# Kernel tuning notes

Measured on AMD Instinct MI355X. Metric: run time of the kernel, lower is better.

The kernel has to match this reference:

```python
import jax, jax.numpy as jnp
import numpy as np

NUM_WIRES = 14
LAYERS = 3
PPL = 3
BATCH = 1024
DIM = 2 ** NUM_WIRES


def setup_inputs() -> dict:
    key = jax.random.key(0)
    k1, k2, k3, k4, k5 = jax.random.split(key, 5)
    sr = jax.random.normal(k1, (BATCH, DIM), jnp.float32)
    si = jax.random.normal(k2, (BATCH, DIM), jnp.float32)
    norm = jnp.sqrt(jnp.sum(sr * sr + si * si, axis=1, keepdims=True))
    sr, si = sr / norm, si / norm  # normalized amplitude-encoded states
    weights = jax.random.normal(k3, (LAYERS, PPL, NUM_WIRES), jnp.float32)
    head_w = jax.random.normal(k4, (1, NUM_WIRES), jnp.float32) / np.sqrt(NUM_WIRES)
    head_b = jax.random.normal(k5, (1,), jnp.float32) * 0.01
    return {"state_real": sr, "state_imag": si, "weights": weights,
            "head_w": head_w, "head_b": head_b}


def _apply_ry_all(st, angles):
    # st: (B,)+(2,)*n complex; apply RY(angles[q]) on each wire q (RYs on distinct wires commute)
    half = angles * 0.5
    c, s = jnp.cos(half), jnp.sin(half)
    for q in range(NUM_WIRES):
        ax = 1 + q
        a0 = jnp.take(st, 0, axis=ax)
        a1 = jnp.take(st, 1, axis=ax)
        n0 = c[q] * a0 - s[q] * a1
        n1 = s[q] * a0 + c[q] * a1
        st = jnp.stack([n0, n1], axis=ax)
    return st


def _apply_cnot(st, ctrl, tgt):
    # flip target axis only where control bit == 1
    ctrl_ax, tgt_ax = 1 + ctrl, 1 + tgt
    flipped = jnp.flip(st, axis=tgt_ax)
    mask_shape = [1] * (NUM_WIRES + 1)
    mask_shape[ctrl_ax] = 2
    mask = (jnp.arange(2).reshape(mask_shape) == 1)
    return jnp.where(mask, flipped, st)


def _circuit(state, weights):
    # state: (B, DIM) complex64 -> PauliZ expvals (B, NUM_WIRES)
    st = state.reshape((-1,) + (2,) * NUM_WIRES)
    for l in range(LAYERS):
        # sequential RY(w[l,p,q]) for p=0..PPL-1 on wire q compose to RY(sum_p w[l,p,q])
        ang = jnp.sum(weights[l], axis=0)  # (NUM_WIRES,)
        st = _apply_ry_all(st, ang)
        for j in range(NUM_WIRES):
            st = _apply_cnot(st, j, (j + 1) % NUM_WIRES)
    probs = st.real ** 2 + st.imag ** 2  # (B,)+(2,)*n
    probs = probs.reshape(-1, DIM)
    idx = jnp.arange(DIM)
    # PennyLane convention: wire 0 is the most significant bit
    bits = (idx[None, :] >> (NUM_WIRES - 1 - jnp.arange(NUM_WIRES))[:, None]) & 1  # (n, DIM)
    signs = (1 - 2 * bits).astype(probs.dtype)
    return probs @ signs.T  # (B, n)


def reference(state_real, state_imag, weights, head_w, head_b):
    state = jax.lax.complex(state_real, state_imag)
    feats = _circuit(state, weights)  # (B, NUM_WIRES)
    return feats @ head_w[0] + head_b[0]  # (B,)
```

## Files before the change

kernel.cpp:

```cpp
#include <hip/hip_runtime.h>

typedef unsigned int u32;

#define DIM 16384
#define NT  512

__host__ __device__ constexpr u32 swz0(u32 d) {
    u32 b1 = (d >> 4) & 1u;
    u32 b2 = (d >> 7) & 1u;
    u32 b3 = ((d >> 6) ^ (d >> 8)) & 1u;
    return d ^ (b1 << 1) ^ (b2 << 2) ^ (b3 << 3);
}

__host__ __device__ constexpr u32 mmap(u32 y) {
    u32 s = y;
    s ^= s >> 1; s ^= s >> 2; s ^= s >> 4; s ^= s >> 8;
    return (s & 0x1FFFu) | (((s ^ (y >> 13)) & 1u) << 13);
}

__device__ __forceinline__ void rot2(float2& a0, float2& a1, float c, float s) {
    float t0x = s * a1.x, t0y = s * a1.y;
    float t1x = s * a0.x, t1y = s * a0.y;
    float n0x = fmaf(c, a0.x, -t0x), n0y = fmaf(c, a0.y, -t0y);
    float n1x = fmaf(c, a1.x,  t1x), n1y = fmaf(c, a1.y,  t1y);
    a0.x = n0x; a0.y = n0y;
    a1.x = n1x; a1.y = n1y;
}

template<int D>
__device__ __forceinline__ void gate32(float2 (&am)[32], float c, float s) {
    #pragma unroll
    for (int r = 0; r < 32; ++r) if (!(r & D)) rot2(am[r], am[r | D], c, s);
}

template<int L>
__device__ __forceinline__ void passA(int tid, float* smem, float2 (&am)[32]) {
    float4* stv = (float4*)smem;
    const float* angC = smem + 32768;
    const float* angS = smem + 32768 + 48;
    u32 sbase = swz0((u32)tid << 2);
    if (L > 0) {
        #pragma unroll
        for (int h = 0; h < 8; ++h) {
            #pragma unroll
            for (int m = 0; m < 2; ++m) {
                u32 idx = (sbase ^ swz0(((u32)h << 11) | ((u32)m << 1))) >> 1;
                float4 v = stv[idx];
                int r = h * 4 + m * 2;
                am[r]     = make_float2(v.x, v.y);
                am[r + 1] = make_float2(v.z, v.w);
            }
        }
    }
    gate32< 1>(am, angC[L * 16 +  0], angS[L * 16 +  0]);
    gate32< 2>(am, angC[L * 16 +  1], angS[L * 16 +  1]);
    gate32< 4>(am, angC[L * 16 + 11], angS[L * 16 + 11]);
    gate32< 8>(am, angC[L * 16 + 12], angS[L * 16 + 12]);
    gate32<16>(am, angC[L * 16 + 13], angS[L * 16 + 13]);
    #pragma unroll
    for (int h = 0; h < 8; ++h) {
        #pragma unroll
        for (int m = 0; m < 2; ++m) {
            u32 idx = (sbase ^ swz0(((u32)h << 11) | ((u32)m << 1))) >> 1;
            int r = h * 4 + m * 2;
            stv[idx] = make_float4(am[r].x, am[r].y, am[r + 1].x, am[r + 1].y);
        }
    }
    __syncthreads();
}

template<int L>
__device__ __forceinline__ void passB(int tid, float* smem, float2 (&am)[32]) {
    float2* st2 = (float2*)smem;
    const float* angC = smem + 32768;
    const float* angS = smem + 32768 + 48;
    u32 ybase = ((u32)tid & 63u) | (((u32)tid >> 6) << 11);
    u32 sbase = swz0(ybase);
    #pragma unroll
    for (int j = 0; j < 32; ++j) am[j] = st2[sbase ^ swz0((u32)j << 6)];
    gate32< 1>(am, angC[L * 16 +  6], angS[L * 16 +  6]);
    gate32< 2>(am, angC[L * 16 +  7], angS[L * 16 +  7]);
    gate32< 4>(am, angC[L * 16 +  8], angS[L * 16 +  8]);
    gate32< 8>(am, angC[L * 16 +  9], angS[L * 16 +  9]);
    gate32<16>(am, angC[L * 16 + 10], angS[L * 16 + 10]);
    #pragma unroll
    for (int j = 0; j < 32; ++j) st2[sbase ^ swz0((u32)j << 6)] = am[j];
    __syncthreads();
}

template<int L>
__device__ __forceinline__ void passC(int tid, float* smem, float2 (&am)[32],
                                      float& acc, float W0) {
    float2* st2 = (float2*)smem;
    float4* stv = (float4*)smem;
    const float* angC  = smem + 32768;
    const float* angS  = smem + 32768 + 48;
    const float* lutLo = smem + 32768 + 96;
    const float* lutHi = smem + 32768 + 96 + 128;
    u32 ybase = (((u32)tid & 1u) << 1) | (((u32)tid >> 1) << 6);
    u32 sbase = swz0(ybase);
    #pragma unroll
    for (int h = 0; h < 16; ++h) {
        u32 idx = (sbase ^ swz0((u32)h << 2)) >> 1;
        float4 v = stv[idx];
        int r = h * 2;
        am[r]     = make_float2(v.x, v.y);
        am[r + 1] = make_float2(v.z, v.w);
    }
    gate32< 2>(am, angC[L * 16 + 2], angS[L * 16 + 2]);
    gate32< 4>(am, angC[L * 16 + 3], angS[L * 16 + 3]);
    gate32< 8>(am, angC[L * 16 + 4], angS[L * 16 + 4]);
    gate32<16>(am, angC[L * 16 + 5], angS[L * 16 + 5]);
    if (L < 2) {
        __syncthreads();
        u32 pbase = swz0(mmap(ybase));
        #pragma unroll
        for (int h = 0; h < 16; ++h) {
            #pragma unroll
            for (int q = 0; q < 2; ++q) {
                u32 slot = pbase ^ swz0(mmap(((u32)h << 2) | (u32)q));
                st2[slot] = am[h * 2 + q];
            }
        }
        __syncthreads();
    } else {
        u32 myb = mmap(ybase);
        #pragma unroll
        for (int h = 0; h < 16; ++h) {
            #pragma unroll
            for (int q = 0; q < 2; ++q) {
                u32 yp = myb ^ mmap(((u32)h << 2) | (u32)q);
                int r = h * 2 + q;
                float p  = fmaf(am[r].x, am[r].x, am[r].y * am[r].y);
                float wv = W0 - 2.0f * (lutLo[yp & 127u] + lutHi[yp >> 7]);
                acc = fmaf(wv, p, acc);
            }
        }
    }
}

__global__ __launch_bounds__(NT, 2) void qsim_kernel(
    const float* __restrict__ sreal, const float* __restrict__ simag,
    const float* __restrict__ wts,   const float* __restrict__ hw,
    const float* __restrict__ hb,    float* __restrict__ out)
{
    extern __shared__ float smem[];
    float* angC   = smem + 32768;
    float* angS   = angC + 48;
    float* lutLo  = angS + 48;
    float* lutHi  = lutLo + 128;
    float* redbuf = lutHi + 128;

    int tid = threadIdx.x;
    int b   = blockIdx.x;

    const float4* pr = (const float4*)(sreal + (size_t)b * DIM);
    const float4* pi = (const float4*)(simag + (size_t)b * DIM);
    float4 vr[8], vi[8];
    #pragma unroll
    for (int h = 0; h < 8; ++h) {
        vr[h] = pr[(h << 9) | tid];
        vi[h] = pi[(h << 9) | tid];
    }

    if (tid < 42) {
        int l = tid / 14, bb = tid % 14, q = 13 - bb;
        float a = 0.5f * (wts[l * 42 + q] + wts[l * 42 + 14 + q] + wts[l * 42 + 28 + q]);
        angC[l * 16 + bb] = cosf(a);
        angS[l * 16 + bb] = sinf(a);
    } else if (tid >= 64 && tid < 192) {
        int i = tid - 64;
        float ssum = 0.f;
        for (int bb = 0; bb < 7; ++bb) if ((i >> bb) & 1) ssum += hw[13 - bb];
        lutLo[i] = ssum;
    } else if (tid >= 192 && tid < 320) {
        int i = tid - 192;
        float ssum = 0.f;
        for (int bb = 0; bb < 7; ++bb) if ((i >> bb) & 1) ssum += hw[6 - bb];
        lutHi[i] = ssum;
    }

    float2 am[32];
    #pragma unroll
    for (int h = 0; h < 8; ++h) {
        am[h * 4 + 0] = make_float2(vr[h].x, vi[h].x);
        am[h * 4 + 1] = make_float2(vr[h].y, vi[h].y);
        am[h * 4 + 2] = make_float2(vr[h].z, vi[h].z);
        am[h * 4 + 3] = make_float2(vr[h].w, vi[h].w);
    }

    __syncthreads();
    float W0  = lutLo[127] + lutHi[127];
    float acc = 0.f;

    passA<0>(tid, smem, am);
    passB<0>(tid, smem, am);
    passC<0>(tid, smem, am, acc, W0);
    passA<1>(tid, smem, am);
    passB<1>(tid, smem, am);
    passC<1>(tid, smem, am, acc, W0);
    passA<2>(tid, smem, am);
    passB<2>(tid, smem, am);
    passC<2>(tid, smem, am, acc, W0);

    #pragma unroll
    for (int off = 32; off > 0; off >>= 1) acc += __shfl_xor(acc, off, 64);
    if ((tid & 63) == 0) redbuf[tid >> 6] = acc;
    __syncthreads();
    if (tid == 0) {
        float tot = hb[0];
        #pragma unroll
        for (int i = 0; i < 8; ++i) tot += redbuf[i];
        out[b] = tot;
    }
}

extern "C" void kernel_launch(void* const* d_in, const int* in_sizes, int n_in,
                              void* d_out, int out_size, void* d_ws, size_t ws_size,
                              hipStream_t stream)
{
    const float* sreal = (const float*)d_in[0];
    const float* simag = (const float*)d_in[1];
    const float* wts   = (const float*)d_in[2];
    const float* hw    = (const float*)d_in[3];
    const float* hb    = (const float*)d_in[4];
    float* out = (float*)d_out;

    int batch = in_sizes[0] / DIM;
    size_t smem_bytes = (32768 + 48 + 48 + 128 + 128 + 16) * sizeof(float);

    (void)hipFuncSetAttribute((const void*)qsim_kernel,
                              hipFuncAttributeMaxDynamicSharedMemorySize, (int)smem_bytes);
    qsim_kernel<<<dim3(batch), dim3(NT), smem_bytes, stream>>>(sreal, simag, wts, hw, hb, out);
}
```

Measured before the change: 211.7 us.

## Process two batch states per block, interleaving gate math with LDS shuffles

Each block now handles two batch rows. It alternates them so one state's register gate math overlaps the other's shared-memory transpose phases, and the batch grid is halved. The rotation math moves to packed v_pk_mul/v_pk_fma instructions on float pairs. The cost is twice the register state per thread, with 64 float2 amplitudes under launch_bounds(512,2), which risks spills. It also adds many more __syncthreads barriers and fewer blocks.

```diff
diff --git a/kernel.cpp b/kernel.cpp
--- a/kernel.cpp
+++ b/kernel.cpp
@@ -1,6 +1,7 @@
 #include <hip/hip_runtime.h>
 
 typedef unsigned int u32;
+typedef float v2f __attribute__((ext_vector_type(2)));
 
 #define DIM 16384
 #define NT  512
@@ -18,131 +19,142 @@
     return (s & 0x1FFFu) | (((s ^ (y >> 13)) & 1u) << 13);
 }
 
-__device__ __forceinline__ void rot2(float2& a0, float2& a1, float c, float s) {
-    float t0x = s * a1.x, t0y = s * a1.y;
-    float t1x = s * a0.x, t1y = s * a0.y;
-    float n0x = fmaf(c, a0.x, -t0x), n0y = fmaf(c, a0.y, -t0y);
-    float n1x = fmaf(c, a1.x,  t1x), n1y = fmaf(c, a1.y,  t1y);
-    a0.x = n0x; a0.y = n0y;
-    a1.x = n1x; a1.y = n1y;
+__device__ __forceinline__ v2f mkv2(float x, float y) { v2f t; t.x = x; t.y = y; return t; }
+
+__device__ __forceinline__ v2f pk_mul(v2f a, v2f b) {
+    v2f d;
+    asm("v_pk_mul_f32 %0, %1, %2" : "=v"(d) : "v"(a), "v"(b));
+    return d;
+}
+__device__ __forceinline__ v2f pk_fma(v2f a, v2f b, v2f c) {
+    v2f d;
+    asm("v_pk_fma_f32 %0, %1, %2, %3" : "=v"(d) : "v"(a), "v"(b), "v"(c));
+    return d;
+}
+
+__device__ __forceinline__ void rot2(v2f& a0, v2f& a1, v2f cc, v2f ss, v2f ns) {
+    v2f t1 = pk_mul(ss, a0);
+    v2f t0 = pk_mul(ns, a1);
+    a0 = pk_fma(cc, a0, t0);
+    a1 = pk_fma(cc, a1, t1);
 }
 
 template<int D>
-__device__ __forceinline__ void gate32(float2 (&am)[32], float c, float s) {
-    #pragma unroll
-    for (int r = 0; r < 32; ++r) if (!(r & D)) rot2(am[r], am[r | D], c, s);
-}
-
+__device__ __forceinline__ void gate32(v2f (&am)[32], float c, float s) {
+    v2f cc = {c, c}, ss = {s, s}, ns = {-s, -s};
+    #pragma unroll
+    for (int r = 0; r < 32; ++r) if (!(r & D)) rot2(am[r], am[r | D], cc, ss, ns);
+}
+
+__device__ __forceinline__ void rdA(int tid, float* smem, v2f (&am)[32]) {
+    float4* stv = (float4*)smem;
+    u32 sbase = swz0((u32)tid << 2);
+    #pragma unroll
+    for (int h = 0; h < 8; ++h)
+        #pragma unroll
+        for (int m = 0; m < 2; ++m) {
+            u32 idx = (sbase ^ swz0(((u32)h << 11) | ((u32)m << 1))) >> 1;
+            float4 v = stv[idx];
+            int r = h * 4 + m * 2;
+            am[r]     = mkv2(v.x, v.y);
+            am[r + 1] = mkv2(v.z, v.w);
+        }
+}
+__device__ __forceinline__ void wrA(int tid, float* smem, v2f (&am)[32]) {
+    float4* stv = (float4*)smem;
+    u32 sbase = swz0((u32)tid << 2);
+    #pragma unroll
+    for (int h = 0; h < 8; ++h)
+        #pragma unroll
+        for (int m = 0; m < 2; ++m) {
+            u32 idx = (sbase ^ swz0(((u32)h << 11) | ((u32)m << 1))) >> 1;
+            int r = h * 4 + m * 2;
+            stv[idx] = make_float4(am[r].x, am[r].y, am[r + 1].x, am[r + 1].y);
+        }
+}
 template<int L>
-__device__ __forceinline__ void passA(int tid, float* smem, float2 (&am)[32]) {
-    float4* stv = (float4*)smem;
-    const float* angC = smem + 32768;
-    const float* angS = smem + 32768 + 48;
-    u32 sbase = swz0((u32)tid << 2);
-    if (L > 0) {
-        #pragma unroll
-        for (int h = 0; h < 8; ++h) {
-            #pragma unroll
-            for (int m = 0; m < 2; ++m) {
-                u32 idx = (sbase ^ swz0(((u32)h << 11) | ((u32)m << 1))) >> 1;
-                float4 v = stv[idx];
-                int r = h * 4 + m * 2;
-                am[r]     = make_float2(v.x, v.y);
-                am[r + 1] = make_float2(v.z, v.w);
-            }
-        }
-    }
+__device__ __forceinline__ void gatesA(const float* angC, const float* angS, v2f (&am)[32]) {
     gate32< 1>(am, angC[L * 16 +  0], angS[L * 16 +  0]);
     gate32< 2>(am, angC[L * 16 +  1], angS[L * 16 +  1]);
     gate32< 4>(am, angC[L * 16 + 11], angS[L * 16 + 11]);
     gate32< 8>(am, angC[L * 16 + 12], angS[L * 16 + 12]);
     gate32<16>(am, angC[L * 16 + 13], angS[L * 16 + 13]);
-    #pragma unroll
-    for (int h = 0; h < 8; ++h) {
-        #pragma unroll
-        for (int m = 0; m < 2; ++m) {
-            u32 idx = (sbase ^ swz0(((u32)h << 11) | ((u32)m << 1))) >> 1;
-            int r = h * 4 + m * 2;
-            stv[idx] = make_float4(am[r].x, am[r].y, am[r + 1].x, am[r + 1].y);
-        }
-    }
-    __syncthreads();
-}
-
-template<int L>
-__device__ __forceinline__ void passB(int tid, float* smem, float2 (&am)[32]) {
-    float2* st2 = (float2*)smem;
-    const float* angC = smem + 32768;
-    const float* angS = smem + 32768 + 48;
+}
+
+__device__ __forceinline__ void rdB(int tid, float* smem, v2f (&am)[32]) {
+    v2f* st2 = (v2f*)smem;
     u32 ybase = ((u32)tid & 63u) | (((u32)tid >> 6) << 11);
     u32 sbase = swz0(ybase);
     #pragma unroll
     for (int j = 0; j < 32; ++j) am[j] = st2[sbase ^ swz0((u32)j << 6)];
+}
+__device__ __forceinline__ void wrB(int tid, float* smem, v2f (&am)[32]) {
+    v2f* st2 = (v2f*)smem;
+    u32 ybase = ((u32)tid & 63u) | (((u32)tid >> 6) << 11);
+    u32 sbase = swz0(ybase);
+    #pragma unroll
+    for (int j = 0; j < 32; ++j) st2[sbase ^ swz0((u32)j << 6)] = am[j];
+}
+template<int L>
+__device__ __forceinline__ void gatesB(const float* angC, const float* angS, v2f (&am)[32]) {
     gate32< 1>(am, angC[L * 16 +  6], angS[L * 16 +  6]);
     gate32< 2>(am, angC[L * 16 +  7], angS[L * 16 +  7]);
     gate32< 4>(am, angC[L * 16 +  8], angS[L * 16 +  8]);
     gate32< 8>(am, angC[L * 16 +  9], angS[L * 16 +  9]);
     gate32<16>(am, angC[L * 16 + 10], angS[L * 16 + 10]);
-    #pragma unroll
-    for (int j = 0; j < 32; ++j) st2[sbase ^ swz0((u32)j << 6)] = am[j];
-    __syncthreads();
-}
-
-template<int L>
-__device__ __forceinline__ void passC(int tid, float* smem, float2 (&am)[32],
-                                      float& acc, float W0) {
-    float2* st2 = (float2*)smem;
+}
+
+__device__ __forceinline__ void rdC(int tid, float* smem, v2f (&am)[32]) {
     float4* stv = (float4*)smem;
-    const float* angC  = smem + 32768;
-    const float* angS  = smem + 32768 + 48;
-    const float* lutLo = smem + 32768 + 96;
-    const float* lutHi = smem + 32768 + 96 + 128;
     u32 ybase = (((u32)tid & 1u) << 1) | (((u32)tid >> 1) << 6);
     u32 sbase = swz0(ybase);
     #pragma unroll
     for (int h = 0; h < 16; ++h) {
         u32 idx = (sbase ^ swz0((u32)h << 2)) >> 1;
         float4 v = stv[idx];
-        int r = h * 2;
-        am[r]     = make_float2(v.x, v.y);
-        am[r + 1] = make_float2(v.z, v.w);
-    }
+        am[h * 2]     = mkv2(v.x, v.y);
+        am[h * 2 + 1] = mkv2(v.z, v.w);
+    }
+}
+__device__ __forceinline__ void wrCs(int tid, float* smem, v2f (&am)[32]) {
+    v2f* st2 = (v2f*)smem;
+    u32 ybase = (((u32)tid & 1u) << 1) | (((u32)tid >> 1) << 6);
+    u32 pbase = swz0(mmap(ybase));
+    #pragma unroll
+    for (int h = 0; h < 16; ++h)
+        #pragma unroll
+        for (int q = 0; q < 2; ++q) {
+            u32 slot = pbase ^ swz0(mmap(((u32)h << 2) | (u32)q));
+            st2[slot] = am[h * 2 + q];
+        }
+}
+template<int L>
+__device__ __forceinline__ void gatesC(const float* angC, const float* angS, v2f (&am)[32]) {
     gate32< 2>(am, angC[L * 16 + 2], angS[L * 16 + 2]);
     gate32< 4>(am, angC[L * 16 + 3], angS[L * 16 + 3]);
     gate32< 8>(am, angC[L * 16 + 4], angS[L * 16 + 4]);
     gate32<16>(am, angC[L * 16 + 5], angS[L * 16 + 5]);
-    if (L < 2) {
-        __syncthreads();
-        u32 pbase = swz0(mmap(ybase));
-        #pragma unroll
-        for (int h = 0; h < 16; ++h) {
-            #pragma unroll
-            for (int q = 0; q < 2; ++q) {
-                u32 slot = pbase ^ swz0(mmap(((u32)h << 2) | (u32)q));
-                st2[slot] = am[h * 2 + q];
-            }
-        }
-        __syncthreads();
-    } else {
-        u32 myb = mmap(ybase);
-        #pragma unroll
-        for (int h = 0; h < 16; ++h) {
-            #pragma unroll
-            for (int q = 0; q < 2; ++q) {
-                u32 yp = myb ^ mmap(((u32)h << 2) | (u32)q);
-                int r = h * 2 + q;
-                float p  = fmaf(am[r].x, am[r].x, am[r].y * am[r].y);
-                float wv = W0 - 2.0f * (lutLo[yp & 127u] + lutHi[yp >> 7]);
-                acc = fmaf(wv, p, acc);
-            }
-        }
-    }
+}
+__device__ __forceinline__ void measC(int tid, const float* lutLo, const float* lutHi,
+                                      v2f (&am)[32], float& acc, float W0) {
+    u32 ybase = (((u32)tid & 1u) << 1) | (((u32)tid >> 1) << 6);
+    u32 myb = mmap(ybase);
+    #pragma unroll
+    for (int h = 0; h < 16; ++h)
+        #pragma unroll
+        for (int q = 0; q < 2; ++q) {
+            u32 yp = myb ^ mmap(((u32)h << 2) | (u32)q);
+            int r = h * 2 + q;
+            float p  = fmaf(am[r].x, am[r].x, am[r].y * am[r].y);
+            float wv = W0 - 2.0f * (lutLo[yp & 127u] + lutHi[yp >> 7]);
+            acc = fmaf(wv, p, acc);
+        }
 }
 
 __global__ __launch_bounds__(NT, 2) void qsim_kernel(
     const float* __restrict__ sreal, const float* __restrict__ simag,
     const float* __restrict__ wts,   const float* __restrict__ hw,
-    const float* __restrict__ hb,    float* __restrict__ out)
+    const float* __restrict__ hb,    float* __restrict__ out, int batch)
 {
     extern __shared__ float smem[];
     float* angC   = smem + 32768;
@@ -152,15 +164,23 @@
     float* redbuf = lutHi + 128;
 
     int tid = threadIdx.x;
-    int b   = blockIdx.x;
-
-    const float4* pr = (const float4*)(sreal + (size_t)b * DIM);
-    const float4* pi = (const float4*)(simag + (size_t)b * DIM);
-    float4 vr[8], vi[8];
-    #pragma unroll
-    for (int h = 0; h < 8; ++h) {
-        vr[h] = pr[(h << 9) | tid];
-        vi[h] = pi[(h << 9) | tid];
+    int b0  = blockIdx.x * 2;
+    int b1  = (b0 + 1 < batch) ? b0 + 1 : b0;
+
+    v2f am[32], bm[32];
+
+    {
+        const float4* pr = (const float4*)(sreal + (size_t)b0 * DIM);
+        const float4* pi = (const float4*)(simag + (size_t)b0 * DIM);
+        #pragma unroll
+        for (int h = 0; h < 8; ++h) {
+            float4 r = pr[(h << 9) | tid];
+            float4 i = pi[(h << 9) | tid];
+            am[h * 4 + 0] = mkv2(r.x, i.x);
+            am[h * 4 + 1] = mkv2(r.y, i.y);
+            am[h * 4 + 2] = mkv2(r.z, i.z);
+            am[h * 4 + 3] = mkv2(r.w, i.w);
+        }
     }
 
     if (tid < 42) {
@@ -180,38 +200,80 @@
         lutHi[i] = ssum;
     }
 
-    float2 am[32];
-    #pragma unroll
-    for (int h = 0; h < 8; ++h) {
-        am[h * 4 + 0] = make_float2(vr[h].x, vi[h].x);
-        am[h * 4 + 1] = make_float2(vr[h].y, vi[h].y);
-        am[h * 4 + 2] = make_float2(vr[h].z, vi[h].z);
-        am[h * 4 + 3] = make_float2(vr[h].w, vi[h].w);
+    {
+        const float4* pr = (const float4*)(sreal + (size_t)b1 * DIM);
+        const float4* pi = (const float4*)(simag + (size_t)b1 * DIM);
+        #pragma unroll
+        for (int h = 0; h < 8; ++h) {
+            float4 r = pr[(h << 9) | tid];
+            float4 i = pi[(h << 9) | tid];
+            bm[h * 4 + 0] = mkv2(r.x, i.x);
+            bm[h * 4 + 1] = mkv2(r.y, i.y);
+            bm[h * 4 + 2] = mkv2(r.z, i.z);
+            bm[h * 4 + 3] = mkv2(r.w, i.w);
+        }
     }
 
     __syncthreads();
-    float W0  = lutLo[127] + lutHi[127];
-    float acc = 0.f;
-
-    passA<0>(tid, smem, am);
-    passB<0>(tid, smem, am);
-    passC<0>(tid, smem, am, acc, W0);
-    passA<1>(tid, smem, am);
-    passB<1>(tid, smem, am);
-    passC<1>(tid, smem, am, acc, W0);
-    passA<2>(tid, smem, am);
-    passB<2>(tid, smem, am);
-    passC<2>(tid, smem, am, acc, W0);
-
-    #pragma unroll
-    for (int off = 32; off > 0; off >>= 1) acc += __shfl_xor(acc, off, 64);
-    if ((tid & 63) == 0) redbuf[tid >> 6] = acc;
+    float W0   = lutLo[127] + lutHi[127];
+    float accX = 0.f, accY = 0.f;
+
+    #define SYNC __syncthreads()
+
+    gatesA<0>(angC, angS, am);
+    wrA(tid, smem, am);                              SYNC;
+    rdB(tid, smem, am);  gatesA<0>(angC, angS, bm);  SYNC;
+    wrA(tid, smem, bm);                              SYNC;
+    rdB(tid, smem, bm);  gatesB<0>(angC, angS, am);  SYNC;
+    wrB(tid, smem, am);                              SYNC;
+    rdC(tid, smem, am);  gatesB<0>(angC, angS, bm);  SYNC;
+    wrB(tid, smem, bm);                              SYNC;
+    rdC(tid, smem, bm);  gatesC<0>(angC, angS, am);  SYNC;
+    wrCs(tid, smem, am);                             SYNC;
+    rdA(tid, smem, am);  gatesC<0>(angC, angS, bm);  SYNC;
+    wrCs(tid, smem, bm);                             SYNC;
+    rdA(tid, smem, bm);  gatesA<1>(angC, angS, am);  SYNC;
+    wrA(tid, smem, am);                              SYNC;
+    rdB(tid, smem, am);  gatesA<1>(angC, angS, bm);  SYNC;
+    wrA(tid, smem, bm);                              SYNC;
+    rdB(tid, smem, bm);  gatesB<1>(angC, angS, am);  SYNC;
+    wrB(tid, smem, am);                              SYNC;
+    rdC(tid, smem, am);  gatesB<1>(angC, angS, bm);  SYNC;
+    wrB(tid, smem, bm);                              SYNC;
+    rdC(tid, smem, bm);  gatesC<1>(angC, angS, am);  SYNC;
+    wrCs(tid, smem, am);                             SYNC;
+    rdA(tid, smem, am);  gatesC<1>(angC, angS, bm);  SYNC;
+    wrCs(tid, smem, bm);                             SYNC;
+    rdA(tid, smem, bm);  gatesA<2>(angC, angS, am);  SYNC;
+    wrA(tid, smem, am);                              SYNC;
+    rdB(tid, smem, am);  gatesA<2>(angC, angS, bm);  SYNC;
+    wrA(tid, smem, bm);                              SYNC;
+    rdB(tid, smem, bm);  gatesB<2>(angC, angS, am);  SYNC;
+    wrB(tid, smem, am);                              SYNC;
+    rdC(tid, smem, am);  gatesB<2>(angC, angS, bm);  SYNC;
+    wrB(tid, smem, bm);                              SYNC;
+    rdC(tid, smem, bm);
+    gatesC<2>(angC, angS, am);  measC(tid, lutLo, lutHi, am, accX, W0);
+    gatesC<2>(angC, angS, bm);  measC(tid, lutLo, lutHi, bm, accY, W0);
+
+    #undef SYNC
+
+    #pragma unroll
+    for (int off = 32; off > 0; off >>= 1) {
+        accX += __shfl_xor(accX, off, 64);
+        accY += __shfl_xor(accY, off, 64);
+    }
+    if ((tid & 63) == 0) {
+        redbuf[tid >> 6]     = accX;
+        redbuf[8 + (tid >> 6)] = accY;
+    }
     __syncthreads();
     if (tid == 0) {
-        float tot = hb[0];
-        #pragma unroll
-        for (int i = 0; i < 8; ++i) tot += redbuf[i];
-        out[b] = tot;
+        float tx = hb[0], ty = hb[0];
+        #pragma unroll
+        for (int i = 0; i < 8; ++i) { tx += redbuf[i]; ty += redbuf[8 + i]; }
+        out[b0] = tx;
+        if (b0 + 1 < batch) out[b0 + 1] = ty;
     }
 }
 
@@ -226,10 +288,11 @@
     const float* hb    = (const float*)d_in[4];
     float* out = (float*)d_out;
 
-    int batch = in_sizes[0] / DIM;
+    int batch  = in_sizes[0] / DIM;
+    int nblk   = (batch + 1) / 2;
     size_t smem_bytes = (32768 + 48 + 48 + 128 + 128 + 16) * sizeof(float);
 
     (void)hipFuncSetAttribute((const void*)qsim_kernel,
                               hipFuncAttributeMaxDynamicSharedMemorySize, (int)smem_bytes);
-    qsim_kernel<<<dim3(batch), dim3(NT), smem_bytes, stream>>>(sreal, simag, wts, hw, hb, out);
-}
+    qsim_kernel<<<dim3(nblk), dim3(NT), smem_bytes, stream>>>(sreal, simag, wts, hw, hb, out, batch);
+}
```

Result: slower. 228.2 us (+7.8%).

## Fold CNOT permutation into per-layer shared-memory address map, removing extra barrier

Applied to the files above, without the earlier changes.

Rather than physically permuting the state through shared memory at the end of passC (which needed an extra __syncthreads before the scatter), each layer now uses a composed address map sig<L> = swizzle∘imap1^L. Threads write amplitudes in place and later passes read them through the permuted index. A modified swizzle (swzN) keeps bank conflicts down, and layer 0 keeps float4 accesses by conditionally swapping pairs. Layers 1 and 2 fall back to scalar float2 LDS accesses, which raises instruction count in exchange for dropping one barrier per layer.

```diff
diff --git a/kernel.cpp b/kernel.cpp
--- a/kernel.cpp
+++ b/kernel.cpp
@@ -5,17 +5,32 @@
 #define DIM 16384
 #define NT  512
 
-__host__ __device__ constexpr u32 swz0(u32 d) {
+__host__ __device__ constexpr u32 swzN(u32 d) {
+    u32 b0 = ((d >> 4) ^ (d >> 5)) & 1u;
     u32 b1 = (d >> 4) & 1u;
-    u32 b2 = (d >> 7) & 1u;
+    u32 b2 = ((d >> 7) ^ (d >> 8)) & 1u;
     u32 b3 = ((d >> 6) ^ (d >> 8)) & 1u;
-    return d ^ (b1 << 1) ^ (b2 << 2) ^ (b3 << 3);
+    return d ^ b0 ^ (b1 << 1) ^ (b2 << 2) ^ (b3 << 3);
 }
 
 __host__ __device__ constexpr u32 mmap(u32 y) {
     u32 s = y;
     s ^= s >> 1; s ^= s >> 2; s ^= s >> 4; s ^= s >> 8;
     return (s & 0x1FFFu) | (((s ^ (y >> 13)) & 1u) << 13);
+}
+
+__host__ __device__ constexpr u32 imap1(u32 z) {
+    u32 lo  = (z ^ (z >> 1)) & 0x0FFFu;
+    u32 y13 = (z ^ (z >> 13)) & 1u;
+    u32 y12 = ((z >> 12) & 1u) ^ y13;
+    return lo | (y12 << 12) | (y13 << 13);
+}
+
+template<int L>
+__host__ __device__ constexpr u32 sig(u32 y) {
+    if constexpr (L == 0) return swzN(y);
+    else if constexpr (L == 1) return swzN(imap1(y));
+    else return swzN(imap1(imap1(y)));
 }
 
 __device__ __forceinline__ void rot2(float2& a0, float2& a1, float c, float s) {
@@ -35,36 +50,50 @@
 
 template<int L>
 __device__ __forceinline__ void passA(int tid, float* smem, float2 (&am)[32]) {
-    float4* stv = (float4*)smem;
+    float2* st2 = (float2*)smem;
     const float* angC = smem + 32768;
     const float* angS = smem + 32768 + 48;
-    u32 sbase = swz0((u32)tid << 2);
     if (L > 0) {
-        #pragma unroll
-        for (int h = 0; h < 8; ++h) {
-            #pragma unroll
-            for (int m = 0; m < 2; ++m) {
-                u32 idx = (sbase ^ swz0(((u32)h << 11) | ((u32)m << 1))) >> 1;
-                float4 v = stv[idx];
-                int r = h * 4 + m * 2;
-                am[r]     = make_float2(v.x, v.y);
-                am[r + 1] = make_float2(v.z, v.w);
-            }
-        }
+        u32 base = sig<L>((u32)tid << 2);
+        #pragma unroll
+        for (int h = 0; h < 8; ++h)
+            #pragma unroll
+            for (int m = 0; m < 2; ++m)
+                #pragma unroll
+                for (int q = 0; q < 2; ++q)
+                    am[h * 4 + m * 2 + q] =
+                        st2[base ^ sig<L>(((u32)h << 11) | ((u32)m << 1) | (u32)q)];
     }
     gate32< 1>(am, angC[L * 16 +  0], angS[L * 16 +  0]);
     gate32< 2>(am, angC[L * 16 +  1], angS[L * 16 +  1]);
     gate32< 4>(am, angC[L * 16 + 11], angS[L * 16 + 11]);
     gate32< 8>(am, angC[L * 16 + 12], angS[L * 16 + 12]);
     gate32<16>(am, angC[L * 16 + 13], angS[L * 16 + 13]);
-    #pragma unroll
-    for (int h = 0; h < 8; ++h) {
-        #pragma unroll
-        for (int m = 0; m < 2; ++m) {
-            u32 idx = (sbase ^ swz0(((u32)h << 11) | ((u32)m << 1))) >> 1;
-            int r = h * 4 + m * 2;
-            stv[idx] = make_float4(am[r].x, am[r].y, am[r + 1].x, am[r + 1].y);
-        }
+    if (L == 0) {
+        float4* stv = (float4*)smem;
+        u32 base = swzN((u32)tid << 2);
+        bool sw = (((tid >> 2) ^ (tid >> 3)) & 1) != 0;
+        #pragma unroll
+        for (int h = 0; h < 8; ++h)
+            #pragma unroll
+            for (int m = 0; m < 2; ++m) {
+                u32 idx = (base ^ swzN(((u32)h << 11) | ((u32)m << 1))) >> 1;
+                int r = h * 4 + m * 2;
+                float2 a0 = am[r], a1 = am[r + 1];
+                float4 v = sw ? make_float4(a1.x, a1.y, a0.x, a0.y)
+                              : make_float4(a0.x, a0.y, a1.x, a1.y);
+                stv[idx] = v;
+            }
+    } else {
+        u32 base = sig<L>((u32)tid << 2);
+        #pragma unroll
+        for (int h = 0; h < 8; ++h)
+            #pragma unroll
+            for (int m = 0; m < 2; ++m)
+                #pragma unroll
+                for (int q = 0; q < 2; ++q)
+                    st2[base ^ sig<L>(((u32)h << 11) | ((u32)m << 1) | (u32)q)] =
+                        am[h * 4 + m * 2 + q];
     }
     __syncthreads();
 }
@@ -75,16 +104,16 @@
     const float* angC = smem + 32768;
     const float* angS = smem + 32768 + 48;
     u32 ybase = ((u32)tid & 63u) | (((u32)tid >> 6) << 11);
-    u32 sbase = swz0(ybase);
-    #pragma unroll
-    for (int j = 0; j < 32; ++j) am[j] = st2[sbase ^ swz0((u32)j << 6)];
+    u32 base = sig<L>(ybase);
+    #pragma unroll
+    for (int j = 0; j < 32; ++j) am[j] = st2[base ^ sig<L>((u32)j << 6)];
     gate32< 1>(am, angC[L * 16 +  6], angS[L * 16 +  6]);
     gate32< 2>(am, angC[L * 16 +  7], angS[L * 16 +  7]);
     gate32< 4>(am, angC[L * 16 +  8], angS[L * 16 +  8]);
     gate32< 8>(am, angC[L * 16 +  9], angS[L * 16 +  9]);
     gate32<16>(am, angC[L * 16 + 10], angS[L * 16 + 10]);
     #pragma unroll
-    for (int j = 0; j < 32; ++j) st2[sbase ^ swz0((u32)j << 6)] = am[j];
+    for (int j = 0; j < 32; ++j) st2[base ^ sig<L>((u32)j << 6)] = am[j];
     __syncthreads();
 }
 
@@ -98,35 +127,57 @@
     const float* lutLo = smem + 32768 + 96;
     const float* lutHi = smem + 32768 + 96 + 128;
     u32 ybase = (((u32)tid & 1u) << 1) | (((u32)tid >> 1) << 6);
-    u32 sbase = swz0(ybase);
-    #pragma unroll
-    for (int h = 0; h < 16; ++h) {
-        u32 idx = (sbase ^ swz0((u32)h << 2)) >> 1;
-        float4 v = stv[idx];
-        int r = h * 2;
-        am[r]     = make_float2(v.x, v.y);
-        am[r + 1] = make_float2(v.z, v.w);
+    if (L == 0) {
+        u32 base = swzN(ybase);
+        #pragma unroll
+        for (int h = 0; h < 16; ++h) {
+            u32 idx = (base ^ swzN((u32)h << 2)) >> 1;
+            float4 v = stv[idx];
+            if (((h >> 2) ^ (h >> 3)) & 1) {
+                am[h * 2 + 1] = make_float2(v.x, v.y);
+                am[h * 2]     = make_float2(v.z, v.w);
+            } else {
+                am[h * 2]     = make_float2(v.x, v.y);
+                am[h * 2 + 1] = make_float2(v.z, v.w);
+            }
+        }
+    } else {
+        u32 base = sig<L>(ybase);
+        #pragma unroll
+        for (int h = 0; h < 16; ++h)
+            #pragma unroll
+            for (int q = 0; q < 2; ++q)
+                am[h * 2 + q] = st2[base ^ sig<L>(((u32)h << 2) | (u32)q)];
     }
     gate32< 2>(am, angC[L * 16 + 2], angS[L * 16 + 2]);
     gate32< 4>(am, angC[L * 16 + 3], angS[L * 16 + 3]);
     gate32< 8>(am, angC[L * 16 + 4], angS[L * 16 + 4]);
     gate32<16>(am, angC[L * 16 + 5], angS[L * 16 + 5]);
     if (L < 2) {
-        __syncthreads();
-        u32 pbase = swz0(mmap(ybase));
-        #pragma unroll
-        for (int h = 0; h < 16; ++h) {
-            #pragma unroll
-            for (int q = 0; q < 2; ++q) {
-                u32 slot = pbase ^ swz0(mmap(((u32)h << 2) | (u32)q));
-                st2[slot] = am[h * 2 + q];
-            }
+        if (L == 0) {
+            u32 base = swzN(ybase);
+            #pragma unroll
+            for (int h = 0; h < 16; ++h) {
+                u32 idx = (base ^ swzN((u32)h << 2)) >> 1;
+                float2 a0 = am[h * 2], a1 = am[h * 2 + 1];
+                if (((h >> 2) ^ (h >> 3)) & 1)
+                    stv[idx] = make_float4(a1.x, a1.y, a0.x, a0.y);
+                else
+                    stv[idx] = make_float4(a0.x, a0.y, a1.x, a1.y);
+            }
+        } else {
+            u32 base = sig<L>(ybase);
+            #pragma unroll
+            for (int h = 0; h < 16; ++h)
+                #pragma unroll
+                for (int q = 0; q < 2; ++q)
+                    st2[base ^ sig<L>(((u32)h << 2) | (u32)q)] = am[h * 2 + q];
         }
         __syncthreads();
     } else {
         u32 myb = mmap(ybase);
         #pragma unroll
-        for (int h = 0; h < 16; ++h) {
+        for (int h = 0; h < 16; ++h)
             #pragma unroll
             for (int q = 0; q < 2; ++q) {
                 u32 yp = myb ^ mmap(((u32)h << 2) | (u32)q);
@@ -135,7 +186,6 @@
                 float wv = W0 - 2.0f * (lutLo[yp & 127u] + lutHi[yp >> 7]);
                 acc = fmaf(wv, p, acc);
             }
-        }
     }
 }
 
```

New measurement: 217.8 us. +2.9%, slower.

## Apply gates in a fixed basis with parity-conjugated rotations, fewer shared-memory passes

Applied to the files above, without the earlier changes.

Replaces the per-layer three-pass scheme, which permuted the state in shared memory after every CNOT ladder, with seven fused passes. Later-layer RY gates are applied directly in the original index basis as rotations on XOR-combined pair offsets, with sign flips given by compile-time parity masks. This removes the separate permutation write/sync steps and packs gates from adjacent layers into the same register pass. It also adds a new swizzle with per-thread float4 half-swapping to avoid bank conflicts. The cost is more complex index maths and per-gate sign selects.

```diff
diff --git a/kernel.cpp b/kernel.cpp
--- a/kernel.cpp
+++ b/kernel.cpp
@@ -5,17 +5,46 @@
 #define DIM 16384
 #define NT  512
 
-__host__ __device__ constexpr u32 swz0(u32 d) {
+__host__ __device__ constexpr u32 swzN(u32 d) {
+    u32 b0 = ((d >> 4) ^ (d >> 5)) & 1u;
     u32 b1 = (d >> 4) & 1u;
-    u32 b2 = (d >> 7) & 1u;
+    u32 b2 = ((d >> 7) ^ (d >> 8)) & 1u;
     u32 b3 = ((d >> 6) ^ (d >> 8)) & 1u;
-    return d ^ (b1 << 1) ^ (b2 << 2) ^ (b3 << 3);
+    return d ^ b0 ^ (b1 << 1) ^ (b2 << 2) ^ (b3 << 3);
 }
 
 __host__ __device__ constexpr u32 mmap(u32 y) {
     u32 s = y;
     s ^= s >> 1; s ^= s >> 2; s ^= s >> 4; s ^= s >> 8;
     return (s & 0x1FFFu) | (((s ^ (y >> 13)) & 1u) << 13);
+}
+
+__host__ __device__ constexpr u32 mpow(u32 x, int L) {
+    for (int i = 0; i < L; ++i) x = mmap(x);
+    return x;
+}
+
+constexpr u32 PV3[5] = {0x040, 0x080, 0x100, 0x200, 0x400};
+constexpr u32 PV4[5] = {0x006, 0x00C, 0x018, 0x030, 0x060};
+constexpr u32 PV5[5] = {0x3001, 0x0003, 0x0C00, 0x1800, 0x3000};
+constexpr u32 PV6[5] = {0x005, 0x00A, 0x014, 0x028, 0x050};
+constexpr u32 PV7[5] = {0x0A0, 0x140, 0x280, 0x500, 0xA00};
+
+__host__ __device__ constexpr u32 moff(const u32* v, int r) {
+    u32 m = 0;
+    for (int i = 0; i < 5; ++i) if ((r >> i) & 1) m ^= v[i];
+    return m;
+}
+__host__ __device__ constexpr u32 parmask(const u32* v, int L, int b) {
+    u32 pm = 0;
+    for (int r = 0; r < 32; ++r)
+        pm |= ((mpow(moff(v, r), L) >> b) & 1u) << r;
+    return pm;
+}
+__host__ __device__ constexpr int hbit(int D) {
+    int h = 0;
+    while (D >> (h + 1)) ++h;
+    return 1 << h;
 }
 
 __device__ __forceinline__ void rot2(float2& a0, float2& a1, float c, float s) {
@@ -27,116 +56,16 @@
     a1.x = n1x; a1.y = n1y;
 }
 
-template<int D>
-__device__ __forceinline__ void gate32(float2 (&am)[32], float c, float s) {
-    #pragma unroll
-    for (int r = 0; r < 32; ++r) if (!(r & D)) rot2(am[r], am[r | D], c, s);
-}
-
-template<int L>
-__device__ __forceinline__ void passA(int tid, float* smem, float2 (&am)[32]) {
-    float4* stv = (float4*)smem;
-    const float* angC = smem + 32768;
-    const float* angS = smem + 32768 + 48;
-    u32 sbase = swz0((u32)tid << 2);
-    if (L > 0) {
-        #pragma unroll
-        for (int h = 0; h < 8; ++h) {
-            #pragma unroll
-            for (int m = 0; m < 2; ++m) {
-                u32 idx = (sbase ^ swz0(((u32)h << 11) | ((u32)m << 1))) >> 1;
-                float4 v = stv[idx];
-                int r = h * 4 + m * 2;
-                am[r]     = make_float2(v.x, v.y);
-                am[r + 1] = make_float2(v.z, v.w);
-            }
-        }
-    }
-    gate32< 1>(am, angC[L * 16 +  0], angS[L * 16 +  0]);
-    gate32< 2>(am, angC[L * 16 +  1], angS[L * 16 +  1]);
-    gate32< 4>(am, angC[L * 16 + 11], angS[L * 16 + 11]);
-    gate32< 8>(am, angC[L * 16 + 12], angS[L * 16 + 12]);
-    gate32<16>(am, angC[L * 16 + 13], angS[L * 16 + 13]);
-    #pragma unroll
-    for (int h = 0; h < 8; ++h) {
-        #pragma unroll
-        for (int m = 0; m < 2; ++m) {
-            u32 idx = (sbase ^ swz0(((u32)h << 11) | ((u32)m << 1))) >> 1;
-            int r = h * 4 + m * 2;
-            stv[idx] = make_float4(am[r].x, am[r].y, am[r + 1].x, am[r + 1].y);
-        }
-    }
-    __syncthreads();
-}
-
-template<int L>
-__device__ __forceinline__ void passB(int tid, float* smem, float2 (&am)[32]) {
-    float2* st2 = (float2*)smem;
-    const float* angC = smem + 32768;
-    const float* angS = smem + 32768 + 48;
-    u32 ybase = ((u32)tid & 63u) | (((u32)tid >> 6) << 11);
-    u32 sbase = swz0(ybase);
-    #pragma unroll
-    for (int j = 0; j < 32; ++j) am[j] = st2[sbase ^ swz0((u32)j << 6)];
-    gate32< 1>(am, angC[L * 16 +  6], angS[L * 16 +  6]);
-    gate32< 2>(am, angC[L * 16 +  7], angS[L * 16 +  7]);
-    gate32< 4>(am, angC[L * 16 +  8], angS[L * 16 +  8]);
-    gate32< 8>(am, angC[L * 16 +  9], angS[L * 16 +  9]);
-    gate32<16>(am, angC[L * 16 + 10], angS[L * 16 + 10]);
-    #pragma unroll
-    for (int j = 0; j < 32; ++j) st2[sbase ^ swz0((u32)j << 6)] = am[j];
-    __syncthreads();
-}
-
-template<int L>
-__device__ __forceinline__ void passC(int tid, float* smem, float2 (&am)[32],
-                                      float& acc, float W0) {
-    float2* st2 = (float2*)smem;
-    float4* stv = (float4*)smem;
-    const float* angC  = smem + 32768;
-    const float* angS  = smem + 32768 + 48;
-    const float* lutLo = smem + 32768 + 96;
-    const float* lutHi = smem + 32768 + 96 + 128;
-    u32 ybase = (((u32)tid & 1u) << 1) | (((u32)tid >> 1) << 6);
-    u32 sbase = swz0(ybase);
-    #pragma unroll
-    for (int h = 0; h < 16; ++h) {
-        u32 idx = (sbase ^ swz0((u32)h << 2)) >> 1;
-        float4 v = stv[idx];
-        int r = h * 2;
-        am[r]     = make_float2(v.x, v.y);
-        am[r + 1] = make_float2(v.z, v.w);
-    }
-    gate32< 2>(am, angC[L * 16 + 2], angS[L * 16 + 2]);
-    gate32< 4>(am, angC[L * 16 + 3], angS[L * 16 + 3]);
-    gate32< 8>(am, angC[L * 16 + 4], angS[L * 16 + 4]);
-    gate32<16>(am, angC[L * 16 + 5], angS[L * 16 + 5]);
-    if (L < 2) {
-        __syncthreads();
-        u32 pbase = swz0(mmap(ybase));
-        #pragma unroll
-        for (int h = 0; h < 16; ++h) {
-            #pragma unroll
-            for (int q = 0; q < 2; ++q) {
-                u32 slot = pbase ^ swz0(mmap(((u32)h << 2) | (u32)q));
-                st2[slot] = am[h * 2 + q];
-            }
-        }
-        __syncthreads();
-    } else {
-        u32 myb = mmap(ybase);
-        #pragma unroll
-        for (int h = 0; h < 16; ++h) {
-            #pragma unroll
-            for (int q = 0; q < 2; ++q) {
-                u32 yp = myb ^ mmap(((u32)h << 2) | (u32)q);
-                int r = h * 2 + q;
-                float p  = fmaf(am[r].x, am[r].x, am[r].y * am[r].y);
-                float wv = W0 - 2.0f * (lutLo[yp & 127u] + lutHi[yp >> 7]);
-                acc = fmaf(wv, p, acc);
-            }
-        }
-    }
+template<int D, u32 PM>
+__device__ __forceinline__ void gateGM(float2 (&am)[32], float c, float s, u32 sB) {
+    constexpr int H = hbit(D);
+    float sp = sB ? -s : s;
+    #pragma unroll
+    for (int r = 0; r < 32; ++r)
+        if (!(r & H)) {
+            if ((PM >> r) & 1) rot2(am[r], am[r ^ D], c, -sp);
+            else               rot2(am[r], am[r ^ D], c,  sp);
+        }
 }
 
 __global__ __launch_bounds__(NT, 2) void qsim_kernel(
@@ -150,6 +79,8 @@
     float* lutLo  = angS + 48;
     float* lutHi  = lutLo + 128;
     float* redbuf = lutHi + 128;
+    float2* st2 = (float2*)smem;
+    float4* stv = (float4*)smem;
 
     int tid = threadIdx.x;
     int b   = blockIdx.x;
@@ -193,15 +124,148 @@
     float W0  = lutLo[127] + lutHi[127];
     float acc = 0.f;
 
-    passA<0>(tid, smem, am);
-    passB<0>(tid, smem, am);
-    passC<0>(tid, smem, am, acc, W0);
-    passA<1>(tid, smem, am);
-    passB<1>(tid, smem, am);
-    passC<1>(tid, smem, am, acc, W0);
-    passA<2>(tid, smem, am);
-    passB<2>(tid, smem, am);
-    passC<2>(tid, smem, am, acc, W0);
+    {
+        gateGM< 1, 0>(am, angC[ 0], angS[ 0], 0);
+        gateGM< 2, 0>(am, angC[ 1], angS[ 1], 0);
+        gateGM< 4, 0>(am, angC[11], angS[11], 0);
+        gateGM< 8, 0>(am, angC[12], angS[12], 0);
+        gateGM<16, 0>(am, angC[13], angS[13], 0);
+        u32 base = swzN((u32)tid << 2);
+        bool sw = (((tid >> 2) ^ (tid >> 3)) & 1) != 0;
+        #pragma unroll
+        for (int h = 0; h < 8; ++h)
+            #pragma unroll
+            for (int m = 0; m < 2; ++m) {
+                u32 idx = (base ^ swzN(((u32)h << 11) | ((u32)m << 1))) >> 1;
+                int r = h * 4 + m * 2;
+                float2 a0 = am[r], a1 = am[r + 1];
+                stv[idx] = sw ? make_float4(a1.x, a1.y, a0.x, a0.y)
+                              : make_float4(a0.x, a0.y, a1.x, a1.y);
+            }
+        __syncthreads();
+    }
+
+    {
+        u32 yb = (((u32)tid & 1u) << 1) | (((u32)tid >> 1) << 6);
+        u32 base = swzN(yb);
+        #pragma unroll
+        for (int h = 0; h < 16; ++h) {
+            u32 idx = (base ^ swzN((u32)h << 2)) >> 1;
+            float4 v = stv[idx];
+            if (((h >> 2) ^ (h >> 3)) & 1) {
+                am[h * 2 + 1] = make_float2(v.x, v.y);
+                am[h * 2]     = make_float2(v.z, v.w);
+            } else {
+                am[h * 2]     = make_float2(v.x, v.y);
+                am[h * 2 + 1] = make_float2(v.z, v.w);
+            }
+        }
+        gateGM< 2, 0>(am, angC[2], angS[2], 0);
+        gateGM< 4, 0>(am, angC[3], angS[3], 0);
+        gateGM< 8, 0>(am, angC[4], angS[4], 0);
+        gateGM<16, 0>(am, angC[5], angS[5], 0);
+        #pragma unroll
+        for (int h = 0; h < 16; ++h) {
+            u32 idx = (base ^ swzN((u32)h << 2)) >> 1;
+            float2 a0 = am[h * 2], a1 = am[h * 2 + 1];
+            if (((h >> 2) ^ (h >> 3)) & 1) stv[idx] = make_float4(a1.x, a1.y, a0.x, a0.y);
+            else                           stv[idx] = make_float4(a0.x, a0.y, a1.x, a1.y);
+        }
+        __syncthreads();
+    }
+
+    {
+        u32 B = ((u32)tid & 63u) | (((u32)tid >> 6) << 11);
+        u32 base = swzN(B);
+        #pragma unroll
+        for (int j = 0; j < 32; ++j) am[j] = st2[base ^ swzN((u32)j << 6)];
+        gateGM< 1, 0>(am, angC[ 6], angS[ 6], 0);
+        gateGM< 2, 0>(am, angC[ 7], angS[ 7], 0);
+        gateGM< 4, 0>(am, angC[ 8], angS[ 8], 0);
+        gateGM< 8, 0>(am, angC[ 9], angS[ 9], 0);
+        gateGM<16, 0>(am, angC[10], angS[10], 0);
+        u32 z1 = mmap(B);
+        gateGM< 3, parmask(PV3, 1,  7)>(am, angC[16 +  7], angS[16 +  7], (z1 >>  7) & 1u);
+        gateGM< 6, parmask(PV3, 1,  8)>(am, angC[16 +  8], angS[16 +  8], (z1 >>  8) & 1u);
+        gateGM<12, parmask(PV3, 1,  9)>(am, angC[16 +  9], angS[16 +  9], (z1 >>  9) & 1u);
+        gateGM<24, parmask(PV3, 1, 10)>(am, angC[16 + 10], angS[16 + 10], (z1 >> 10) & 1u);
+        #pragma unroll
+        for (int j = 0; j < 32; ++j) st2[base ^ swzN((u32)j << 6)] = am[j];
+        __syncthreads();
+    }
+
+    {
+        u32 B = ((u32)tid & 3u) | (((u32)tid >> 2) << 7);
+        u32 base = swzN(B);
+        #pragma unroll
+        for (int r = 0; r < 32; ++r) am[r] = st2[base ^ swzN(moff(PV4, r))];
+        u32 z1 = mmap(B);
+        gateGM< 1, parmask(PV4, 1, 2)>(am, angC[16 + 2], angS[16 + 2], (z1 >> 2) & 1u);
+        gateGM< 2, parmask(PV4, 1, 3)>(am, angC[16 + 3], angS[16 + 3], (z1 >> 3) & 1u);
+        gateGM< 4, parmask(PV4, 1, 4)>(am, angC[16 + 4], angS[16 + 4], (z1 >> 4) & 1u);
+        gateGM< 8, parmask(PV4, 1, 5)>(am, angC[16 + 5], angS[16 + 5], (z1 >> 5) & 1u);
+        gateGM<16, parmask(PV4, 1, 6)>(am, angC[16 + 6], angS[16 + 6], (z1 >> 6) & 1u);
+        #pragma unroll
+        for (int r = 0; r < 32; ++r) st2[base ^ swzN(moff(PV4, r))] = am[r];
+        __syncthreads();
+    }
+
+    {
+        u32 B = (((u32)tid & 0xFFu) << 2) | (((u32)tid >> 8) << 13);
+        u32 base = swzN(B);
+        #pragma unroll
+        for (int r = 0; r < 32; ++r) am[r] = st2[base ^ swzN(moff(PV5, r))];
+        u32 z1 = mmap(B), z2 = mmap(z1);
+        gateGM< 1, parmask(PV5, 1,  0)>(am, angC[16 +  0], angS[16 +  0], (z1 >>  0) & 1u);
+        gateGM< 2, parmask(PV5, 1,  1)>(am, angC[16 +  1], angS[16 +  1], (z1 >>  1) & 1u);
+        gateGM< 4, parmask(PV5, 1, 11)>(am, angC[16 + 11], angS[16 + 11], (z1 >> 11) & 1u);
+        gateGM< 8, parmask(PV5, 1, 12)>(am, angC[16 + 12], angS[16 + 12], (z1 >> 12) & 1u);
+        gateGM<16, parmask(PV5, 1, 13)>(am, angC[16 + 13], angS[16 + 13], (z1 >> 13) & 1u);
+        gateGM<25, parmask(PV5, 2,  0)>(am, angC[32 +  0], angS[32 +  0], (z2 >>  0) & 1u);
+        gateGM< 3, parmask(PV5, 2,  1)>(am, angC[32 +  1], angS[32 +  1], (z2 >>  1) & 1u);
+        gateGM<12, parmask(PV5, 2, 12)>(am, angC[32 + 12], angS[32 + 12], (z2 >> 12) & 1u);
+        gateGM<24, parmask(PV5, 2, 13)>(am, angC[32 + 13], angS[32 + 13], (z2 >> 13) & 1u);
+        #pragma unroll
+        for (int r = 0; r < 32; ++r) st2[base ^ swzN(moff(PV5, r))] = am[r];
+        __syncthreads();
+    }
+
+    {
+        u32 B = ((u32)tid & 3u) | (((u32)tid >> 2) << 7);
+        u32 base = swzN(B);
+        #pragma unroll
+        for (int r = 0; r < 32; ++r) am[r] = st2[base ^ swzN(moff(PV6, r))];
+        u32 z2 = mpow(B, 2);
+        gateGM< 1, parmask(PV6, 2, 2)>(am, angC[32 + 2], angS[32 + 2], (z2 >> 2) & 1u);
+        gateGM< 2, parmask(PV6, 2, 3)>(am, angC[32 + 3], angS[32 + 3], (z2 >> 3) & 1u);
+        gateGM< 4, parmask(PV6, 2, 4)>(am, angC[32 + 4], angS[32 + 4], (z2 >> 4) & 1u);
+        gateGM< 8, parmask(PV6, 2, 5)>(am, angC[32 + 5], angS[32 + 5], (z2 >> 5) & 1u);
+        gateGM<16, parmask(PV6, 2, 6)>(am, angC[32 + 6], angS[32 + 6], (z2 >> 6) & 1u);
+        #pragma unroll
+        for (int r = 0; r < 32; ++r) st2[base ^ swzN(moff(PV6, r))] = am[r];
+        __syncthreads();
+    }
+
+    {
+        u32 B = ((u32)tid & 0x7Fu) | (((u32)tid >> 7) << 12);
+        u32 base = swzN(B);
+        #pragma unroll
+        for (int r = 0; r < 32; ++r) am[r] = st2[base ^ swzN(moff(PV7, r))];
+        u32 z2 = mpow(B, 2);
+        gateGM< 1, parmask(PV7, 2,  7)>(am, angC[32 +  7], angS[32 +  7], (z2 >>  7) & 1u);
+        gateGM< 2, parmask(PV7, 2,  8)>(am, angC[32 +  8], angS[32 +  8], (z2 >>  8) & 1u);
+        gateGM< 4, parmask(PV7, 2,  9)>(am, angC[32 +  9], angS[32 +  9], (z2 >>  9) & 1u);
+        gateGM< 8, parmask(PV7, 2, 10)>(am, angC[32 + 10], angS[32 + 10], (z2 >> 10) & 1u);
+        gateGM<16, parmask(PV7, 2, 11)>(am, angC[32 + 11], angS[32 + 11], (z2 >> 11) & 1u);
+        u32 wB = mmap(z2);
+        #pragma unroll
+        for (int r = 0; r < 32; ++r) {
+            u32 w = wB ^ mpow(moff(PV7, r), 3);
+            float p  = fmaf(am[r].x, am[r].x, am[r].y * am[r].y);
+            float wv = W0 - 2.0f * (lutLo[w & 127u] + lutHi[w >> 7]);
+            acc = fmaf(wv, p, acc);
+        }
+    }
 
     #pragma unroll
     for (int off = 32; off > 0; off >>= 1) acc += __shfl_xor(acc, off, 64);
```

New measurement: 208.9 us. Within noise of the previous version (-1.3%).
